# Kernel optimization log

Measured on AMD Instinct MI355X. Metric: run time of the kernel, lower is better.

Reference implementation:

```python
import jax, jax.numpy as jnp
import numpy as np
from jax import lax

WIN = 7
K1, K2 = 0.01, 0.03
THRESH = 5e-05  # brain threshold
NP_WIN = WIN * WIN
COV_NORM = NP_WIN / (NP_WIN - 1)


def _erode(m, k):
    # cv2.erode default border value is +inf -> SAME padding with +inf init
    return lax.reduce_window(m, jnp.inf, lax.min, (1, k, k), (1, 1, 1), 'SAME')


def _dilate(m, k):
    # cv2.dilate default border value is -inf -> SAME padding with -inf init
    return lax.reduce_window(m, -jnp.inf, lax.max, (1, k, k), (1, 1, 1), 'SAME')


def make_mask(Y):
    # threshold -> erode x1 (3x3) -> dilate x15 (== 31x31) -> erode x14 (== 29x29)
    m = (Y > THRESH).astype(Y.dtype)
    m = _erode(m, 3)
    m = _dilate(m, 2 * 15 + 1)
    m = _erode(m, 2 * 14 + 1)
    return m


def _box_mean(x):
    # valid 7x7 box filter on [B,H,W] -> [B,H-6,W-6]
    s = lax.reduce_window(x, jnp.float32(0.0), lax.add, (1, WIN, WIN), (1, 1, 1), 'VALID')
    return s / NP_WIN


def setup_inputs() -> dict:
    key = jax.random.key(0)
    kx, ky = jax.random.split(key)
    B, H, W = 128, 384, 384
    X = jax.random.uniform(kx, (B, H, W), dtype=jnp.float32)
    Y = jax.random.uniform(ky, (B, H, W), dtype=jnp.float32)
    data_range = jnp.ones((B,), dtype=jnp.float32)
    return {"X": X, "Y": Y, "data_range": data_range}


def reference(X, Y, data_range):
    mask = make_mask(Y)
    Xm = X * mask
    Ym = Y * mask
    dr = data_range[:, None, None]  # broadcast over valid-window output [B,H',W']
    C1 = (K1 * dr) ** 2
    C2 = (K2 * dr) ** 2
    ux = _box_mean(Xm)
    uy = _box_mean(Ym)
    uxx = _box_mean(Xm * Xm)
    uyy = _box_mean(Ym * Ym)
    uxy = _box_mean(Xm * Ym)
    vx = COV_NORM * (uxx - ux * ux)
    vy = COV_NORM * (uyy - uy * uy)
    vxy = COV_NORM * (uxy - ux * uy)
    A1 = 2 * ux * uy + C1
    A2 = 2 * vxy + C2
    B1 = ux * ux + uy * uy + C1
    B2 = vx + vy + C2
    S = (A1 * A2) / (B1 * B2)
    return 1 - S.mean()
```

## Files before the change

### kernel.cpp

```cpp
#include <hip/hip_runtime.h>
#include <stdint.h>

typedef unsigned long long u64;
typedef float v2 __attribute__((ext_vector_type(2)));

#define THRESH_F 5e-5f
#define BB 128
#define HH 384
#define WW_ 384
#define WPR 6
#define IMG_WORDS (HH*WPR)
#define OH 378
#define OW 378
#define PIX (BB*HH*WW_)
#define COVN (49.0f/48.0f)

#define SLAB 48
#define HALO 30
#define MAXROWS (SLAB + 2*HALO)
#define MAXW (MAXROWS * WPR)

#define BIN_BLOCKS 1536

__device__ __forceinline__ int div6(int w) { return (w * 43691) >> 18; }

__global__ void __launch_bounds__(256) k_binarize(const float* __restrict__ Y,
                                                  u64* __restrict__ bits,
                                                  float* __restrict__ accum) {
    if (blockIdx.x == 0) {
        for (int i = threadIdx.x; i < 1024; i += 256) accum[i] = 0.f;
    }
    const int lane = threadIdx.x & 63;
    const int wave = (blockIdx.x * 256 + threadIdx.x) >> 6;
    const int nwaves = BIN_BLOCKS * 4;
    const int NSTEP = PIX / 256;
    for (int s = wave; s < NSTEP; s += nwaves) {
        size_t base = (size_t)s * 256 + lane;
        float a0 = Y[base];
        float a1 = Y[base + 64];
        float a2 = Y[base + 128];
        float a3 = Y[base + 192];
        u64 b0 = __ballot(a0 > THRESH_F);
        u64 b1 = __ballot(a1 > THRESH_F);
        u64 b2 = __ballot(a2 > THRESH_F);
        u64 b3 = __ballot(a3 > THRESH_F);
        if (lane < 4) {
            u64 v = (lane == 0) ? b0 : (lane == 1) ? b1 : (lane == 2) ? b2 : b3;
            bits[(size_t)s * 4 + lane] = v;
        }
    }
}

__global__ void __launch_bounds__(256) k_morph(const u64* __restrict__ gbits,
                                               u64* __restrict__ gout_all) {
    __shared__ u64 A[MAXW];
    __shared__ u64 Bf[MAXW];
    const int blk = blockIdx.x;
    const int b = blk >> 3;
    const int slab = blk & 7;
    const int r0 = slab * SLAB;
    const int w0row = (r0 - HALO < 0) ? 0 : r0 - HALO;
    int w1row = r0 + SLAB + HALO; if (w1row > HH) w1row = HH;
    const int nrows = w1row - w0row;
    const int NW = nrows * WPR;
    const int t = threadIdx.x;

    const u64* gin = gbits + (size_t)b * IMG_WORDS + (size_t)w0row * WPR;
    for (int w = t; w < NW; w += 256) A[w] = gin[w];
    __syncthreads();

    for (int w = t; w < NW; w += 256) {
        int row = div6(w);
        int ww = w - row * 6;
        int rlo = row > 0 ? row - 1 : row;
        int rhi = row < nrows - 1 ? row + 1 : row;
        u64 res = ~0ull;
        for (int rr = rlo; rr <= rhi; ++rr) {
            const u64* rp = &A[rr * 6];
            u64 a = ww > 0 ? rp[ww - 1] : 0ull;
            u64 bb = rp[ww];
            u64 c = ww < 5 ? rp[ww + 1] : 0ull;
            u64 l  = (bb << 1) | (ww > 0 ? (a >> 63) : 1ull);
            u64 r2 = (bb >> 1) | (ww < 5 ? (c << 63) : (1ull << 63));
            res &= bb & l & r2;
        }
        Bf[w] = res;
    }
    __syncthreads();

    for (int w = t; w < NW; w += 256) {
        int row = div6(w);
        int ww = w - row * 6;
        const u64* rp = &Bf[row * 6];
        u64 a = ww > 0 ? rp[ww - 1] : 0ull;
        u64 bb = rp[ww];
        u64 c = ww < 5 ? rp[ww + 1] : 0ull;
        __uint128_t X = (((__uint128_t)bb) << 64) | a;
        X |= X << 1; X |= X << 2; X |= X << 4; X |= X << 8;
        __uint128_t Z = (((__uint128_t)c) << 64) | bb;
        Z |= Z >> 1; Z |= Z >> 2; Z |= Z >> 4; Z |= Z >> 8;
        A[w] = (u64)(X >> 64) | (u64)Z;
    }
    __syncthreads();

    for (int w = t; w < NW; w += 256) {
        int row = div6(w);
        int ww = w - row * 6;
        int lo2 = row - 15 < 0 ? 0 : row - 15;
        int hi2 = row + 15 > nrows - 1 ? nrows - 1 : row + 15;
        u64 acc = 0ull;
        for (int rr = lo2; rr <= hi2; ++rr) acc |= A[rr * 6 + ww];
        Bf[w] = acc;
    }
    __syncthreads();

    for (int w = t; w < NW; w += 256) {
        int row = div6(w);
        int ww = w - row * 6;
        const u64* rp = &Bf[row * 6];
        u64 a = ww > 0 ? rp[ww - 1] : ~0ull;
        u64 bb = rp[ww];
        u64 c = ww < 5 ? rp[ww + 1] : ~0ull;
        u64 na = ~a, nb = ~bb, nc = ~c;
        __uint128_t X = (((__uint128_t)nb) << 64) | na;
        X |= X << 1; X |= X << 2; X |= X << 4; X |= X << 7;
        __uint128_t Z = (((__uint128_t)nc) << 64) | nb;
        Z |= Z >> 1; Z |= Z >> 2; Z |= Z >> 4; Z |= Z >> 7;
        A[w] = ~((u64)(X >> 64) | (u64)Z);
    }
    __syncthreads();

    u64* gout = gout_all + (size_t)b * IMG_WORDS;
    const int base = r0 - w0row;
    for (int w = t; w < SLAB * WPR; w += 256) {
        int lrow = div6(w);
        int ww = w - lrow * 6;
        int lr = base + lrow;
        int lo2 = lr - 14 < 0 ? 0 : lr - 14;
        int hi2 = lr + 14 > nrows - 1 ? nrows - 1 : lr + 14;
        u64 acc = ~0ull;
        for (int rr = lo2; rr <= hi2; ++rr) acc &= A[rr * 6 + ww];
        gout[(size_t)(r0 + lrow) * WPR + ww] = acc;
    }
}

__global__ void __launch_bounds__(128) k_ssim(
    const float* __restrict__ Xg, const float* __restrict__ Yg,
    const float* __restrict__ drg, const u64* __restrict__ Mg,
    float* __restrict__ accum)
{
    const int tx = threadIdx.x & 63;
    const int cz = threadIdx.x >> 6;
    const int p  = blockIdx.x * 64 + tx;
    const int chunk = blockIdx.y * 2 + cz;
    const int b  = blockIdx.z;

    float lsum = 0.0f;
    if (p < 189) {
        const int j  = p * 2;
        const int i0 = chunk * 27;
        const float drv = drg[b];
        const float C1q = 1e-4f * drv * drv * 2401.0f;
        const float C2q = 9e-4f * drv * drv * 2401.0f;
        const float* xr = Xg + (size_t)b * HH * WW_ + (size_t)i0 * WW_ + j;
        const float* yr = Yg + (size_t)b * HH * WW_ + (size_t)i0 * WW_ + j;
        const unsigned* mr = (const unsigned*)Mg + ((size_t)b * HH + i0) * 12 + (j >> 5);
        const int sh32 = j & 31;

        v2 r0[7], r1[7], r2[7], r3[7], r4[7];
        #pragma unroll
        for (int t = 0; t < 7; ++t) {
            r0[t] = 0.f; r1[t] = 0.f; r2[t] = 0.f; r3[t] = 0.f; r4[t] = 0.f;
        }
        v2 s0 = 0.f, s1 = 0.f, s2 = 0.f, s3 = 0.f, s4 = 0.f;

        v2 ax0 = *(const v2*)(xr),     ax1 = *(const v2*)(xr + 2);
        v2 ax2 = *(const v2*)(xr + 4), ax3 = *(const v2*)(xr + 6);
        v2 ay0 = *(const v2*)(yr),     ay1 = *(const v2*)(yr + 2);
        v2 ay2 = *(const v2*)(yr + 4), ay3 = *(const v2*)(yr + 6);
        unsigned am0 = mr[0], am1 = mr[1];

        const float* xn1 = xr + WW_;
        const float* yn1 = yr + WW_;
        v2 bx0 = *(const v2*)(xn1),     bx1 = *(const v2*)(xn1 + 2);
        v2 bx2 = *(const v2*)(xn1 + 4), bx3 = *(const v2*)(xn1 + 6);
        v2 by0 = *(const v2*)(yn1),     by1 = *(const v2*)(yn1 + 2);
        v2 by2 = *(const v2*)(yn1 + 4), by3 = *(const v2*)(yn1 + 6);
        unsigned bm0 = mr[12], bm1 = mr[13];

        for (int bs = 0; bs < 35; bs += 7) {
            #pragma unroll
            for (int ph = 0; ph < 7; ++ph) {
                const int rr = bs + ph;
                if (rr >= 33) break;

                v2 tx0 = 0.f, tx1 = 0.f, tx2 = 0.f, tx3 = 0.f;
                v2 ty0 = 0.f, ty1 = 0.f, ty2 = 0.f, ty3 = 0.f;
                unsigned tm0 = 0u, tm1 = 0u;
                if (rr + 2 < 33) {
                    const float* xn = xr + (size_t)(rr + 2) * WW_;
                    const float* yn = yr + (size_t)(rr + 2) * WW_;
                    tx0 = *(const v2*)(xn);     tx1 = *(const v2*)(xn + 2);
                    tx2 = *(const v2*)(xn + 4); tx3 = *(const v2*)(xn + 6);
                    ty0 = *(const v2*)(yn);     ty1 = *(const v2*)(yn + 2);
                    ty2 = *(const v2*)(yn + 4); ty3 = *(const v2*)(yn + 6);
                    const unsigned* mn = mr + (size_t)(rr + 2) * 12;
                    tm0 = mn[0]; tm1 = mn[1];
                }

                unsigned win8 = __builtin_amdgcn_alignbit(am1, am0, sh32) & 0xFFu;
                v2 xa = ax0, xb = ax1, xc = ax2, xd = ax3;
                v2 ya = ay0, yb = ay1, yc = ay2, yd = ay3;

                if (__builtin_expect(__any(win8 != 0xFFu), 0)) {
                    float m0 = (float)( win8       & 1u);
                    float m1 = (float)((win8 >> 1) & 1u);
                    float m2 = (float)((win8 >> 2) & 1u);
                    float m3 = (float)((win8 >> 3) & 1u);
                    float m4 = (float)((win8 >> 4) & 1u);
                    float m5 = (float)((win8 >> 5) & 1u);
                    float m6 = (float)((win8 >> 6) & 1u);
                    float m7 = (float)((win8 >> 7) & 1u);
                    xa.x *= m0; xa.y *= m1; xb.x *= m2; xb.y *= m3;
                    xc.x *= m4; xc.y *= m5; xd.x *= m6; xd.y *= m7;
                    ya.x *= m0; ya.y *= m1; yb.x *= m2; yb.y *= m3;
                    yc.x *= m4; yc.y *= m5; yd.x *= m6; yd.y *= m7;
                }

                v2 xxa = xa * xa, xxb = xb * xb, xxc = xc * xc, xxd = xd * xd;
                v2 yya = ya * ya, yyb = yb * yb, yyc = yc * yc, yyd = yd * yd;
                v2 xya = xa * ya, xyb = xb * yb, xyc = xc * yc, xyd = xd * yd;

                float h;
                h = ((xa.x + xa.y) + (xb.x + xb.y)) + ((xc.x + xc.y) + xd.x);
                v2 hX  = { h, h + xd.y - xa.x };
                h = ((ya.x + ya.y) + (yb.x + yb.y)) + ((yc.x + yc.y) + yd.x);
                v2 hY  = { h, h + yd.y - ya.x };
                h = ((xxa.x + xxa.y) + (xxb.x + xxb.y)) + ((xxc.x + xxc.y) + xxd.x);
                v2 hXX = { h, h + xxd.y - xxa.x };
                h = ((yya.x + yya.y) + (yyb.x + yyb.y)) + ((yyc.x + yyc.y) + yyd.x);
                v2 hYY = { h, h + yyd.y - yya.x };
                h = ((xya.x + xya.y) + (xyb.x + xyb.y)) + ((xyc.x + xyc.y) + xyd.x);
                v2 hXY = { h, h + xyd.y - xya.x };

                v2 o;
                o = r0[ph]; r0[ph] = hX;  s0 += hX  - o;
                o = r1[ph]; r1[ph] = hY;  s1 += hY  - o;
                o = r2[ph]; r2[ph] = hXX; s2 += hXX - o;
                o = r3[ph]; r3[ph] = hYY; s3 += hYY - o;
                o = r4[ph]; r4[ph] = hXY; s4 += hXY - o;

                if (rr >= 6) {
                    v2 t3  = s0 * s1;
                    v2 t12 = s1 * s1 + s0 * s0;
                    v2 A1  = 2.0f * t3 + C1q;
                    v2 u   = 49.0f * s4 - t3;
                    v2 A2  = (2.0f * COVN) * u + C2q;
                    v2 B1  = t12 + C1q;
                    v2 w   = s2 + s3;
                    v2 vsum = 49.0f * w - t12;
                    v2 B2  = COVN * vsum + C2q;
                    v2 num = A1 * A2;
                    v2 den = B1 * B2;
                    float q0 = __builtin_amdgcn_rcpf(den.x);
                    float q1 = __builtin_amdgcn_rcpf(den.y);
                    lsum += num.x * q0 + num.y * q1;
                }

                ax0 = bx0; ax1 = bx1; ax2 = bx2; ax3 = bx3;
                ay0 = by0; ay1 = by1; ay2 = by2; ay3 = by3;
                am0 = bm0; am1 = bm1;
                bx0 = tx0; bx1 = tx1; bx2 = tx2; bx3 = tx3;
                by0 = ty0; by1 = ty1; by2 = ty2; by3 = ty3;
                bm0 = tm0; bm1 = tm1;
            }
        }
    }

    #pragma unroll
    for (int off = 32; off > 0; off >>= 1) lsum += __shfl_down(lsum, off);
    if (tx == 0) {
        int flat = ((blockIdx.z * 14 + blockIdx.y * 2 + cz) * 3 + blockIdx.x);
        atomicAdd(&accum[flat & 1023], lsum);
    }
}

__global__ void k_final(const float* __restrict__ accum, float* __restrict__ out) {
    __shared__ double sm[256];
    double v = 0.0;
    for (int i = threadIdx.x; i < 1024; i += 256) v += (double)accum[i];
    sm[threadIdx.x] = v;
    __syncthreads();
    #pragma unroll
    for (int off = 128; off > 0; off >>= 1) {
        if (threadIdx.x < off) sm[threadIdx.x] += sm[threadIdx.x + off];
        __syncthreads();
    }
    if (threadIdx.x == 0) {
        out[0] = (float)(1.0 - sm[0] / 18289152.0);
    }
}

extern "C" void kernel_launch(void* const* d_in, const int* in_sizes, int n_in,
                              void* d_out, int out_size, void* d_ws, size_t ws_size,
                              hipStream_t stream) {
    const float* X  = (const float*)d_in[0];
    const float* Y  = (const float*)d_in[1];
    const float* dr = (const float*)d_in[2];
    float* out = (float*)d_out;

    char* ws = (char*)d_ws;
    float* accum = (float*)ws;
    u64* maskB = (u64*)(ws + 4096);
    u64* bitsRaw = (u64*)(ws + 4096 + (size_t)(BB * IMG_WORDS) * 8);

    k_binarize<<<BIN_BLOCKS, 256, 0, stream>>>(Y, bitsRaw, accum);
    k_morph<<<BB * 8, 256, 0, stream>>>(bitsRaw, maskB);
    dim3 g(3, 7, 128);
    k_ssim<<<g, 128, 0, stream>>>(X, Y, dr, maskB, accum);
    k_final<<<1, 256, 0, stream>>>(accum, out);
}
```

Baseline: 215.4 us.

## Fuse thresholding into morphology kernel and make prefetch loads unconditional

```diff
diff --git a/kernel.cpp b/kernel.cpp
--- a/kernel.cpp
+++ b/kernel.cpp
@@ -20,39 +20,11 @@
 #define MAXROWS (SLAB + 2*HALO)
 #define MAXW (MAXROWS * WPR)
 
-#define BIN_BLOCKS 1536
-
 __device__ __forceinline__ int div6(int w) { return (w * 43691) >> 18; }
 
-__global__ void __launch_bounds__(256) k_binarize(const float* __restrict__ Y,
-                                                  u64* __restrict__ bits,
-                                                  float* __restrict__ accum) {
-    if (blockIdx.x == 0) {
-        for (int i = threadIdx.x; i < 1024; i += 256) accum[i] = 0.f;
-    }
-    const int lane = threadIdx.x & 63;
-    const int wave = (blockIdx.x * 256 + threadIdx.x) >> 6;
-    const int nwaves = BIN_BLOCKS * 4;
-    const int NSTEP = PIX / 256;
-    for (int s = wave; s < NSTEP; s += nwaves) {
-        size_t base = (size_t)s * 256 + lane;
-        float a0 = Y[base];
-        float a1 = Y[base + 64];
-        float a2 = Y[base + 128];
-        float a3 = Y[base + 192];
-        u64 b0 = __ballot(a0 > THRESH_F);
-        u64 b1 = __ballot(a1 > THRESH_F);
-        u64 b2 = __ballot(a2 > THRESH_F);
-        u64 b3 = __ballot(a3 > THRESH_F);
-        if (lane < 4) {
-            u64 v = (lane == 0) ? b0 : (lane == 1) ? b1 : (lane == 2) ? b2 : b3;
-            bits[(size_t)s * 4 + lane] = v;
-        }
-    }
-}
-
-__global__ void __launch_bounds__(256) k_morph(const u64* __restrict__ gbits,
-                                               u64* __restrict__ gout_all) {
+__global__ void __launch_bounds__(256) k_morph(const float* __restrict__ Yg,
+                                               u64* __restrict__ gout_all,
+                                               float* __restrict__ accum) {
     __shared__ u64 A[MAXW];
     __shared__ u64 Bf[MAXW];
     const int blk = blockIdx.x;
@@ -65,8 +37,29 @@
     const int NW = nrows * WPR;
     const int t = threadIdx.x;
 
-    const u64* gin = gbits + (size_t)b * IMG_WORDS + (size_t)w0row * WPR;
-    for (int w = t; w < NW; w += 256) A[w] = gin[w];
+    if (blk == 0) {
+        for (int i = t; i < 1024; i += 256) accum[i] = 0.f;
+    }
+
+    {
+        const int lane = t & 63;
+        const int wv = t >> 6;
+        const float* yb = Yg + (size_t)b * (HH * WW_) + (size_t)w0row * WW_;
+        for (int base = wv * 4; base < NW; base += 16) {
+            float a0 = yb[(size_t)(base + 0) * 64 + lane];
+            float a1 = yb[(size_t)(base + 1) * 64 + lane];
+            float a2 = yb[(size_t)(base + 2) * 64 + lane];
+            float a3 = yb[(size_t)(base + 3) * 64 + lane];
+            u64 w0 = __ballot(a0 > THRESH_F);
+            u64 w1 = __ballot(a1 > THRESH_F);
+            u64 w2 = __ballot(a2 > THRESH_F);
+            u64 w3 = __ballot(a3 > THRESH_F);
+            if (lane == 0) {
+                A[base + 0] = w0; A[base + 1] = w1;
+                A[base + 2] = w2; A[base + 3] = w3;
+            }
+        }
+    }
     __syncthreads();
 
     for (int w = t; w < NW; w += 256) {
@@ -194,19 +187,15 @@
                 const int rr = bs + ph;
                 if (rr >= 33) break;
 
-                v2 tx0 = 0.f, tx1 = 0.f, tx2 = 0.f, tx3 = 0.f;
-                v2 ty0 = 0.f, ty1 = 0.f, ty2 = 0.f, ty3 = 0.f;
-                unsigned tm0 = 0u, tm1 = 0u;
-                if (rr + 2 < 33) {
-                    const float* xn = xr + (size_t)(rr + 2) * WW_;
-                    const float* yn = yr + (size_t)(rr + 2) * WW_;
-                    tx0 = *(const v2*)(xn);     tx1 = *(const v2*)(xn + 2);
-                    tx2 = *(const v2*)(xn + 4); tx3 = *(const v2*)(xn + 6);
-                    ty0 = *(const v2*)(yn);     ty1 = *(const v2*)(yn + 2);
-                    ty2 = *(const v2*)(yn + 4); ty3 = *(const v2*)(yn + 6);
-                    const unsigned* mn = mr + (size_t)(rr + 2) * 12;
-                    tm0 = mn[0]; tm1 = mn[1];
-                }
+                int rp = rr + 2; if (rp > 32) rp = 32;
+                const float* xn = xr + (size_t)rp * WW_;
+                const float* yn = yr + (size_t)rp * WW_;
+                v2 tx0 = *(const v2*)(xn),     tx1 = *(const v2*)(xn + 2);
+                v2 tx2 = *(const v2*)(xn + 4), tx3 = *(const v2*)(xn + 6);
+                v2 ty0 = *(const v2*)(yn),     ty1 = *(const v2*)(yn + 2);
+                v2 ty2 = *(const v2*)(yn + 4), ty3 = *(const v2*)(yn + 6);
+                const unsigned* mn = mr + (size_t)rp * 12;
+                unsigned tm0 = mn[0], tm1 = mn[1];
 
                 unsigned win8 = __builtin_amdgcn_alignbit(am1, am0, sh32) & 0xFFu;
                 v2 xa = ax0, xb = ax1, xc = ax2, xd = ax3;
@@ -312,10 +301,8 @@
     char* ws = (char*)d_ws;
     float* accum = (float*)ws;
     u64* maskB = (u64*)(ws + 4096);
-    u64* bitsRaw = (u64*)(ws + 4096 + (size_t)(BB * IMG_WORDS) * 8);
-
-    k_binarize<<<BIN_BLOCKS, 256, 0, stream>>>(Y, bitsRaw, accum);
-    k_morph<<<BB * 8, 256, 0, stream>>>(bitsRaw, maskB);
+
+    k_morph<<<BB * 8, 256, 0, stream>>>(Y, maskB, accum);
     dim3 g(3, 7, 128);
     k_ssim<<<g, 128, 0, stream>>>(X, Y, dr, maskB, accum);
     k_final<<<1, 256, 0, stream>>>(accum, out);
```

Result: slower. 221.3 us (+2.8%).

## Fuse final reduction into SSIM kernel via last-wave counter and fully unroll row loop

Applied to the files above, without the earlier changes.

```diff
diff --git a/kernel.cpp b/kernel.cpp
--- a/kernel.cpp
+++ b/kernel.cpp
@@ -21,6 +21,7 @@
 #define MAXW (MAXROWS * WPR)
 
 #define BIN_BLOCKS 1536
+#define TOTAL_SSIM_WAVES 5376u
 
 __device__ __forceinline__ int div6(int w) { return (w * 43691) >> 18; }
 
@@ -28,7 +29,7 @@
                                                   u64* __restrict__ bits,
                                                   float* __restrict__ accum) {
     if (blockIdx.x == 0) {
-        for (int i = threadIdx.x; i < 1024; i += 256) accum[i] = 0.f;
+        for (int i = threadIdx.x; i < 1088; i += 256) accum[i] = 0.f;
     }
     const int lane = threadIdx.x & 63;
     const int wave = (blockIdx.x * 256 + threadIdx.x) >> 6;
@@ -147,7 +148,7 @@
 __global__ void __launch_bounds__(128) k_ssim(
     const float* __restrict__ Xg, const float* __restrict__ Yg,
     const float* __restrict__ drg, const u64* __restrict__ Mg,
-    float* __restrict__ accum)
+    float* __restrict__ accum, float* __restrict__ out)
 {
     const int tx = threadIdx.x & 63;
     const int cz = threadIdx.x >> 6;
@@ -188,116 +189,114 @@
         v2 by2 = *(const v2*)(yn1 + 4), by3 = *(const v2*)(yn1 + 6);
         unsigned bm0 = mr[12], bm1 = mr[13];
 
-        for (int bs = 0; bs < 35; bs += 7) {
-            #pragma unroll
-            for (int ph = 0; ph < 7; ++ph) {
-                const int rr = bs + ph;
-                if (rr >= 33) break;
-
-                v2 tx0 = 0.f, tx1 = 0.f, tx2 = 0.f, tx3 = 0.f;
-                v2 ty0 = 0.f, ty1 = 0.f, ty2 = 0.f, ty3 = 0.f;
-                unsigned tm0 = 0u, tm1 = 0u;
-                if (rr + 2 < 33) {
-                    const float* xn = xr + (size_t)(rr + 2) * WW_;
-                    const float* yn = yr + (size_t)(rr + 2) * WW_;
-                    tx0 = *(const v2*)(xn);     tx1 = *(const v2*)(xn + 2);
-                    tx2 = *(const v2*)(xn + 4); tx3 = *(const v2*)(xn + 6);
-                    ty0 = *(const v2*)(yn);     ty1 = *(const v2*)(yn + 2);
-                    ty2 = *(const v2*)(yn + 4); ty3 = *(const v2*)(yn + 6);
-                    const unsigned* mn = mr + (size_t)(rr + 2) * 12;
-                    tm0 = mn[0]; tm1 = mn[1];
-                }
-
-                unsigned win8 = __builtin_amdgcn_alignbit(am1, am0, sh32) & 0xFFu;
-                v2 xa = ax0, xb = ax1, xc = ax2, xd = ax3;
-                v2 ya = ay0, yb = ay1, yc = ay2, yd = ay3;
-
-                if (__builtin_expect(__any(win8 != 0xFFu), 0)) {
-                    float m0 = (float)( win8       & 1u);
-                    float m1 = (float)((win8 >> 1) & 1u);
-                    float m2 = (float)((win8 >> 2) & 1u);
-                    float m3 = (float)((win8 >> 3) & 1u);
-                    float m4 = (float)((win8 >> 4) & 1u);
-                    float m5 = (float)((win8 >> 5) & 1u);
-                    float m6 = (float)((win8 >> 6) & 1u);
-                    float m7 = (float)((win8 >> 7) & 1u);
-                    xa.x *= m0; xa.y *= m1; xb.x *= m2; xb.y *= m3;
-                    xc.x *= m4; xc.y *= m5; xd.x *= m6; xd.y *= m7;
-                    ya.x *= m0; ya.y *= m1; yb.x *= m2; yb.y *= m3;
-                    yc.x *= m4; yc.y *= m5; yd.x *= m6; yd.y *= m7;
-                }
-
-                v2 xxa = xa * xa, xxb = xb * xb, xxc = xc * xc, xxd = xd * xd;
-                v2 yya = ya * ya, yyb = yb * yb, yyc = yc * yc, yyd = yd * yd;
-                v2 xya = xa * ya, xyb = xb * yb, xyc = xc * yc, xyd = xd * yd;
-
-                float h;
-                h = ((xa.x + xa.y) + (xb.x + xb.y)) + ((xc.x + xc.y) + xd.x);
-                v2 hX  = { h, h + xd.y - xa.x };
-                h = ((ya.x + ya.y) + (yb.x + yb.y)) + ((yc.x + yc.y) + yd.x);
-                v2 hY  = { h, h + yd.y - ya.x };
-                h = ((xxa.x + xxa.y) + (xxb.x + xxb.y)) + ((xxc.x + xxc.y) + xxd.x);
-                v2 hXX = { h, h + xxd.y - xxa.x };
-                h = ((yya.x + yya.y) + (yyb.x + yyb.y)) + ((yyc.x + yyc.y) + yyd.x);
-                v2 hYY = { h, h + yyd.y - yya.x };
-                h = ((xya.x + xya.y) + (xyb.x + xyb.y)) + ((xyc.x + xyc.y) + xyd.x);
-                v2 hXY = { h, h + xyd.y - xya.x };
-
-                v2 o;
-                o = r0[ph]; r0[ph] = hX;  s0 += hX  - o;
-                o = r1[ph]; r1[ph] = hY;  s1 += hY  - o;
-                o = r2[ph]; r2[ph] = hXX; s2 += hXX - o;
-                o = r3[ph]; r3[ph] = hYY; s3 += hYY - o;
-                o = r4[ph]; r4[ph] = hXY; s4 += hXY - o;
-
-                if (rr >= 6) {
-                    v2 t3  = s0 * s1;
-                    v2 t12 = s1 * s1 + s0 * s0;
-                    v2 A1  = 2.0f * t3 + C1q;
-                    v2 u   = 49.0f * s4 - t3;
-                    v2 A2  = (2.0f * COVN) * u + C2q;
-                    v2 B1  = t12 + C1q;
-                    v2 w   = s2 + s3;
-                    v2 vsum = 49.0f * w - t12;
-                    v2 B2  = COVN * vsum + C2q;
-                    v2 num = A1 * A2;
-                    v2 den = B1 * B2;
-                    float q0 = __builtin_amdgcn_rcpf(den.x);
-                    float q1 = __builtin_amdgcn_rcpf(den.y);
-                    lsum += num.x * q0 + num.y * q1;
-                }
-
-                ax0 = bx0; ax1 = bx1; ax2 = bx2; ax3 = bx3;
-                ay0 = by0; ay1 = by1; ay2 = by2; ay3 = by3;
-                am0 = bm0; am1 = bm1;
-                bx0 = tx0; bx1 = tx1; bx2 = tx2; bx3 = tx3;
-                by0 = ty0; by1 = ty1; by2 = ty2; by3 = ty3;
-                bm0 = tm0; bm1 = tm1;
+        #pragma unroll
+        for (int rr = 0; rr < 33; ++rr) {
+            const int ph = rr % 7;
+
+            v2 tx0 = 0.f, tx1 = 0.f, tx2 = 0.f, tx3 = 0.f;
+            v2 ty0 = 0.f, ty1 = 0.f, ty2 = 0.f, ty3 = 0.f;
+            unsigned tm0 = 0u, tm1 = 0u;
+            if (rr + 2 < 33) {
+                const float* xn = xr + (size_t)(rr + 2) * WW_;
+                const float* yn = yr + (size_t)(rr + 2) * WW_;
+                tx0 = *(const v2*)(xn);     tx1 = *(const v2*)(xn + 2);
+                tx2 = *(const v2*)(xn + 4); tx3 = *(const v2*)(xn + 6);
+                ty0 = *(const v2*)(yn);     ty1 = *(const v2*)(yn + 2);
+                ty2 = *(const v2*)(yn + 4); ty3 = *(const v2*)(yn + 6);
+                const unsigned* mn = mr + (size_t)(rr + 2) * 12;
+                tm0 = mn[0]; tm1 = mn[1];
             }
+
+            unsigned win8 = __builtin_amdgcn_alignbit(am1, am0, sh32) & 0xFFu;
+            v2 xa = ax0, xb = ax1, xc = ax2, xd = ax3;
+            v2 ya = ay0, yb = ay1, yc = ay2, yd = ay3;
+
+            if (__builtin_expect(__any(win8 != 0xFFu), 0)) {
+                float m0 = (float)( win8       & 1u);
+                float m1 = (float)((win8 >> 1) & 1u);
+                float m2 = (float)((win8 >> 2) & 1u);
+                float m3 = (float)((win8 >> 3) & 1u);
+                float m4 = (float)((win8 >> 4) & 1u);
+                float m5 = (float)((win8 >> 5) & 1u);
+                float m6 = (float)((win8 >> 6) & 1u);
+                float m7 = (float)((win8 >> 7) & 1u);
+                xa.x *= m0; xa.y *= m1; xb.x *= m2; xb.y *= m3;
+                xc.x *= m4; xc.y *= m5; xd.x *= m6; xd.y *= m7;
+                ya.x *= m0; ya.y *= m1; yb.x *= m2; yb.y *= m3;
+                yc.x *= m4; yc.y *= m5; yd.x *= m6; yd.y *= m7;
+            }
+
+            v2 xxa = xa * xa, xxb = xb * xb, xxc = xc * xc, xxd = xd * xd;
+            v2 yya = ya * ya, yyb = yb * yb, yyc = yc * yc, yyd = yd * yd;
+            v2 xya = xa * ya, xyb = xb * yb, xyc = xc * yc, xyd = xd * yd;
+
+            float h;
+            h = ((xa.x + xa.y) + (xb.x + xb.y)) + ((xc.x + xc.y) + xd.x);
+            v2 hX  = { h, h + xd.y - xa.x };
+            h = ((ya.x + ya.y) + (yb.x + yb.y)) + ((yc.x + yc.y) + yd.x);
+            v2 hY  = { h, h + yd.y - ya.x };
+            h = ((xxa.x + xxa.y) + (xxb.x + xxb.y)) + ((xxc.x + xxc.y) + xxd.x);
+            v2 hXX = { h, h + xxd.y - xxa.x };
+            h = ((yya.x + yya.y) + (yyb.x + yyb.y)) + ((yyc.x + yyc.y) + yyd.x);
+            v2 hYY = { h, h + yyd.y - yya.x };
+            h = ((xya.x + xya.y) + (xyb.x + xyb.y)) + ((xyc.x + xyc.y) + xyd.x);
+            v2 hXY = { h, h + xyd.y - xya.x };
+
+            v2 o;
+            o = r0[ph]; r0[ph] = hX;  s0 += hX  - o;
+            o = r1[ph]; r1[ph] = hY;  s1 += hY  - o;
+            o = r2[ph]; r2[ph] = hXX; s2 += hXX - o;
+            o = r3[ph]; r3[ph] = hYY; s3 += hYY - o;
+            o = r4[ph]; r4[ph] = hXY; s4 += hXY - o;
+
+            if (rr >= 6) {
+                v2 t3  = s0 * s1;
+                v2 t12 = s1 * s1 + s0 * s0;
+                v2 A1  = 2.0f * t3 + C1q;
+                v2 u   = 49.0f * s4 - t3;
+                v2 A2  = (2.0f * COVN) * u + C2q;
+                v2 B1  = t12 + C1q;
+                v2 w   = s2 + s3;
+                v2 vsum = 49.0f * w - t12;
+                v2 B2  = COVN * vsum + C2q;
+                v2 num = A1 * A2;
+                v2 den = B1 * B2;
+                float q0 = __builtin_amdgcn_rcpf(den.x);
+                float q1 = __builtin_amdgcn_rcpf(den.y);
+                lsum += num.x * q0 + num.y * q1;
+            }
+
+            ax0 = bx0; ax1 = bx1; ax2 = bx2; ax3 = bx3;
+            ay0 = by0; ay1 = by1; ay2 = by2; ay3 = by3;
+            am0 = bm0; am1 = bm1;
+            bx0 = tx0; bx1 = tx1; bx2 = tx2; bx3 = tx3;
+            by0 = ty0; by1 = ty1; by2 = ty2; by3 = ty3;
+            bm0 = tm0; bm1 = tm1;
         }
     }
 
     #pragma unroll
     for (int off = 32; off > 0; off >>= 1) lsum += __shfl_down(lsum, off);
+
+    unsigned old = 0u;
     if (tx == 0) {
         int flat = ((blockIdx.z * 14 + blockIdx.y * 2 + cz) * 3 + blockIdx.x);
         atomicAdd(&accum[flat & 1023], lsum);
-    }
-}
-
-__global__ void k_final(const float* __restrict__ accum, float* __restrict__ out) {
-    __shared__ double sm[256];
-    double v = 0.0;
-    for (int i = threadIdx.x; i < 1024; i += 256) v += (double)accum[i];
-    sm[threadIdx.x] = v;
-    __syncthreads();
-    #pragma unroll
-    for (int off = 128; off > 0; off >>= 1) {
-        if (threadIdx.x < off) sm[threadIdx.x] += sm[threadIdx.x + off];
-        __syncthreads();
-    }
-    if (threadIdx.x == 0) {
-        out[0] = (float)(1.0 - sm[0] / 18289152.0);
+        __threadfence();
+        old = atomicAdd((unsigned*)(accum + 1024), 1u);
+    }
+    old = __shfl(old, 0);
+
+    if (old == TOTAL_SSIM_WAVES - 1u) {
+        double v = 0.0;
+        for (int i = tx; i < 1024; i += 64) {
+            float f = __hip_atomic_load(&accum[i], __ATOMIC_RELAXED,
+                                        __HIP_MEMORY_SCOPE_AGENT);
+            v += (double)f;
+        }
+        #pragma unroll
+        for (int off = 32; off > 0; off >>= 1) v += __shfl_down(v, off);
+        if (tx == 0) out[0] = (float)(1.0 - v / 18289152.0);
     }
 }
 
@@ -311,12 +310,11 @@
 
     char* ws = (char*)d_ws;
     float* accum = (float*)ws;
-    u64* maskB = (u64*)(ws + 4096);
-    u64* bitsRaw = (u64*)(ws + 4096 + (size_t)(BB * IMG_WORDS) * 8);
+    u64* maskB = (u64*)(ws + 8192);
+    u64* bitsRaw = (u64*)(ws + 8192 + (size_t)(BB * IMG_WORDS) * 8);
 
     k_binarize<<<BIN_BLOCKS, 256, 0, stream>>>(Y, bitsRaw, accum);
     k_morph<<<BB * 8, 256, 0, stream>>>(bitsRaw, maskB);
     dim3 g(3, 7, 128);
-    k_ssim<<<g, 128, 0, stream>>>(X, Y, dr, maskB, accum);
-    k_final<<<1, 256, 0, stream>>>(accum, out);
+    k_ssim<<<g, 128, 0, stream>>>(X, Y, dr, maskB, accum, out);
 }
```

After: 379.8 us. 1.76x slower.
